# Kernel tuning notes

Measured on AMD Instinct MI355X. Metric: run time of the kernel, lower is better.

Reference implementation:

```python
import jax, jax.numpy as jnp
import numpy as np

B, G, K, C, NT = 128, 64, 32, 256, 8192


def setup_inputs() -> dict:
    key = jax.random.key(0)
    ks = jax.random.split(key, 8)
    s = lambda fan_in: 1.0 / np.sqrt(fan_in)
    return {
        "patch_features": jax.random.normal(ks[0], (B, G, C), jnp.float32),
        "neighborhood": jax.random.normal(ks[1], (B, G, K, 3), jnp.float32),
        "codebook": jax.random.normal(ks[2], (NT, C), jnp.float32),
        "w1": jax.random.normal(ks[3], (512, C), jnp.float32) * s(C),
        "b1": jnp.zeros((512,), jnp.float32),
        "w2": jax.random.normal(ks[4], (256, 512), jnp.float32) * s(512),
        "b2": jnp.zeros((256,), jnp.float32),
        "w3": jax.random.normal(ks[5], (3 * K, 256), jnp.float32) * s(256),
        "b3": jnp.zeros((3 * K,), jnp.float32),
    }


def reference(patch_features, neighborhood, codebook, w1, b1, w2, b2, w3, b3):
    b, g, c = patch_features.shape
    k = neighborhood.shape[2]
    # squared euclidean distances to codebook (argmin equals argmin of cdist p=2)
    d2 = (
        jnp.sum(patch_features * patch_features, -1, keepdims=True)
        - 2.0 * jnp.einsum("bgc,nc->bgn", patch_features, codebook)
        + jnp.sum(codebook * codebook, -1)
    )  # [B,G,NT]
    token_ids = jnp.argmin(d2, axis=-1)          # [B,G]
    quantized = codebook[token_ids]              # [B,G,C] gather
    # 1x1 Conv1d stack == per-token MLP
    h = jax.nn.relu(jnp.einsum("bgc,oc->bgo", quantized, w1) + b1)
    h = jax.nn.relu(jnp.einsum("bgc,oc->bgo", h, w2) + b2)
    rec = jnp.einsum("bgc,oc->bgo", h, w3) + b3  # [B,G,3K]
    rec = rec.reshape(b * g, k, 3)
    gt = neighborhood.reshape(b * g, k, 3)
    # Chamfer distance L2 (squared) both directions
    diff = rec[:, :, None, :] - gt[:, None, :, :]  # [BG,K,K,3]
    dd = jnp.sum(diff * diff, -1)                  # [BG,K,K]
    loss = jnp.mean(jnp.min(dd, axis=2)) + jnp.mean(jnp.min(dd, axis=1))
    return loss
```

## Files before the change

kernel.cpp:

```cpp
#include <hip/hip_runtime.h>
#include <hip/hip_bf16.h>
#include <float.h>

#define NTOK 8192
#define NCB  8192
#define CDIM 256
#define KPTS 32
#define SQNT 24.0f
#define INV_CFOLD (SQNT * SQNT * 64.0f)

typedef __attribute__((ext_vector_type(8))) short short8;
typedef __attribute__((ext_vector_type(4))) float f32x4;
typedef __attribute__((ext_vector_type(4))) int i32x4;
typedef unsigned int u32;
typedef unsigned long long u64;

__device__ __forceinline__ void gl_lds16(const void* g, void* l) {
  __builtin_amdgcn_global_load_lds(
      (const __attribute__((address_space(1))) u32*)(g),
      (__attribute__((address_space(3))) u32*)(l), 16, 0, 0);
}

__device__ __forceinline__ ushort bf16_rne(float x) {
  u32 u = __float_as_uint(x);
  return (ushort)((u + 0x7fffu + ((u >> 16) & 1u)) >> 16);
}

__device__ __forceinline__ int pack4i8(int a, int b, int c, int d) {
  return (a & 0xff) | ((b & 0xff) << 8) | ((c & 0xff) << 16) | ((d & 0xff) << 24);
}

__global__ __launch_bounds__(256) void prep_k(
    const float* __restrict__ pf, const float* __restrict__ cb,
    const float* __restrict__ w1, const float* __restrict__ w2,
    const float* __restrict__ w3,
    i32x4* __restrict__ pf1, i32x4* __restrict__ pf2,
    i32x4* __restrict__ cb1, i32x4* __restrict__ cb2,
    ushort* __restrict__ cb_bf, ushort* __restrict__ w1s,
    ushort* __restrict__ w2s, ushort* __restrict__ w3s,
    float* __restrict__ cnorm) {
  int gid = blockIdx.x * 4 + (threadIdx.x >> 6);
  int lane = threadIdx.x & 63, r16 = lane & 15, quad = lane >> 4;
  if (gid < 4096) {
    bool is_cb = gid >= 2048;
    int t = is_cb ? gid - 2048 : gid;
    int tile = t >> 2, kb = t & 3;
    const float* src = is_cb ? cb : pf;
    int row = tile * 16 + r16;
    const float* sp = src + (size_t)row * CDIM + kb * 64 + quad * 16;
    float4 v0 = ((const float4*)sp)[0];
    float4 v1 = ((const float4*)sp)[1];
    float4 v2 = ((const float4*)sp)[2];
    float4 v3 = ((const float4*)sp)[3];
    float x[16] = {v0.x, v0.y, v0.z, v0.w, v1.x, v1.y, v1.z, v1.w,
                   v2.x, v2.y, v2.z, v2.w, v3.x, v3.y, v3.z, v3.w};
    int q1[16], q2[16];
    float s = 0.f;
#pragma unroll
    for (int e = 0; e < 16; e++) {
      float as = x[e] * SQNT;
      float a1 = rintf(as);
      a1 = fminf(fmaxf(a1, -127.f), 127.f);
      float a2 = rintf((as - a1) * 128.f);
      a2 = fminf(fmaxf(a2, -127.f), 127.f);
      q1[e] = (int)a1;
      q2[e] = (int)a2;
      s += x[e] * x[e];
    }
    i32x4 p1 = {pack4i8(q1[0], q1[1], q1[2], q1[3]),
                pack4i8(q1[4], q1[5], q1[6], q1[7]),
                pack4i8(q1[8], q1[9], q1[10], q1[11]),
                pack4i8(q1[12], q1[13], q1[14], q1[15])};
    i32x4 p2 = {pack4i8(q2[0], q2[1], q2[2], q2[3]),
                pack4i8(q2[4], q2[5], q2[6], q2[7]),
                pack4i8(q2[8], q2[9], q2[10], q2[11]),
                pack4i8(q2[12], q2[13], q2[14], q2[15])};
    size_t o = (size_t)t * 64 + lane;
    (is_cb ? cb1 : pf1)[o] = p1;
    (is_cb ? cb2 : pf2)[o] = p2;
    if (is_cb) {
      s += __shfl_xor(s, 16, 64);
      s += __shfl_xor(s, 32, 64);
      if (quad == 0) atomicAdd(cnorm + row, s);
    }
  } else if (gid < 8192) {
    int t = gid - 4096;
    int tile = t >> 3, kb = t & 7;
    int row = tile * 16 + r16;
    const float* sp = cb + (size_t)row * CDIM + kb * 32 + quad * 8;
    float4 a = ((const float4*)sp)[0];
    float4 b = ((const float4*)sp)[1];
    short8 vh = {(short)bf16_rne(a.x), (short)bf16_rne(a.y),
                 (short)bf16_rne(a.z), (short)bf16_rne(a.w),
                 (short)bf16_rne(b.x), (short)bf16_rne(b.y),
                 (short)bf16_rne(b.z), (short)bf16_rne(b.w)};
    *(short8*)(cb_bf + ((size_t)tile * 8 + kb) * 512 + lane * 8) = vh;
  } else if (gid < 8752) {
    int t = gid - 8192;
    const float* src;
    ushort* dst;
    int KB;
    if (t < 256)      { src = w1; dst = w1s; KB = 8; }
    else if (t < 512) { src = w2; dst = w2s; KB = 16; t -= 256; }
    else              { src = w3; dst = w3s; KB = 8;  t -= 512; }
    int tile = t / KB, kb = t - tile * KB, K = KB * 32;
    int row = tile * 16 + r16;
    const float* sp = src + (size_t)row * K + kb * 32 + quad * 8;
    float4 a = ((const float4*)sp)[0];
    float4 b = ((const float4*)sp)[1];
    short8 vh = {(short)bf16_rne(a.x), (short)bf16_rne(a.y),
                 (short)bf16_rne(a.z), (short)bf16_rne(a.w),
                 (short)bf16_rne(b.x), (short)bf16_rne(b.y),
                 (short)bf16_rne(b.z), (short)bf16_rne(b.w)};
    *(short8*)(dst + ((size_t)tile * KB + kb) * 512 + lane * 8) = vh;
  }
}

__global__ __launch_bounds__(256, 2) void argmin_k(
    const char* __restrict__ A1g, const char* __restrict__ A2g,
    const char* __restrict__ B1g, const char* __restrict__ B2g,
    const float* __restrict__ cnorm, u64* __restrict__ pkeys) {
  __shared__ char lds[32 * 1024];
  int tid = threadIdx.x;
  int ns = blockIdx.x, mt = blockIdx.y;
  int wv = tid >> 6, lane = tid & 63;
  int quad = lane >> 4, r16 = lane & 15;
  int wr = wv >> 1, wc = wv & 1;

  int bvi[4][4], bii[4][4];
#pragma unroll
  for (int i = 0; i < 4; i++)
#pragma unroll
    for (int r = 0; r < 4; r++) { bvi[i][r] = 0x7fffffff; bii[i][r] = 0x7fffffff; }

  const char* bsrc = (wv == 0) ? A1g : (wv == 1) ? A2g : (wv == 2) ? B1g : B2g;

  for (int nts = 0; nts < 4; ++nts) {
    int nt = ns * 4 + nts;
    i32x4 am[4][4], ac[4][4];
#pragma unroll
    for (int i = 0; i < 4; i++)
#pragma unroll
      for (int j = 0; j < 4; j++) {
        am[i][j] = (i32x4){0, 0, 0, 0};
        ac[i][j] = (i32x4){0, 0, 0, 0};
      }
    for (int kb = 0; kb < 4; ++kb) {
#pragma unroll
      for (int u = 0; u < 8; ++u) {
        int gt = ((wv < 2) ? mt : nt) * 8 + u;
        gl_lds16(bsrc + ((size_t)gt * 4 + kb) * 1024 + lane * 16,
                 lds + (wv * 8 + u) * 1024);
      }
      __syncthreads();
      i32x4 f1[4], f2[4], g1[4], g2[4];
#pragma unroll
      for (int i = 0; i < 4; i++) {
        f1[i] = *(const i32x4*)(lds + (wr * 4 + i) * 1024 + lane * 16);
        f2[i] = *(const i32x4*)(lds + (8 + wr * 4 + i) * 1024 + lane * 16);
      }
#pragma unroll
      for (int j = 0; j < 4; j++) {
        g1[j] = *(const i32x4*)(lds + (16 + wc * 4 + j) * 1024 + lane * 16);
        g2[j] = *(const i32x4*)(lds + (24 + wc * 4 + j) * 1024 + lane * 16);
      }
#pragma unroll
      for (int i = 0; i < 4; i++)
#pragma unroll
        for (int j = 0; j < 4; j++) {
          am[i][j] = __builtin_amdgcn_mfma_i32_16x16x64_i8(f1[i], g1[j], am[i][j], 0, 0, 0);
          ac[i][j] = __builtin_amdgcn_mfma_i32_16x16x64_i8(f1[i], g2[j], ac[i][j], 0, 0, 0);
          ac[i][j] = __builtin_amdgcn_mfma_i32_16x16x64_i8(f2[i], g1[j], ac[i][j], 0, 0, 0);
        }
      __syncthreads();
    }
#pragma unroll
    for (int j = 0; j < 4; j++) {
      int col = nt * 128 + wc * 64 + j * 16 + r16;
      int cni = __float2int_rn(cnorm[col] * INV_CFOLD);
#pragma unroll
      for (int i = 0; i < 4; i++)
#pragma unroll
        for (int r = 0; r < 4; r++) {
          int di = cni - (am[i][j][r] * 128 + ac[i][j][r]);
          if (di < bvi[i][r]) { bvi[i][r] = di; bii[i][r] = col; }
        }
    }
  }
#pragma unroll
  for (int m = 1; m < 16; m <<= 1) {
#pragma unroll
    for (int i = 0; i < 4; i++)
#pragma unroll
      for (int r = 0; r < 4; r++) {
        int ov = __shfl_xor(bvi[i][r], m, 64);
        int oi = __shfl_xor(bii[i][r], m, 64);
        if (ov < bvi[i][r] || (ov == bvi[i][r] && oi < bii[i][r])) {
          bvi[i][r] = ov;
          bii[i][r] = oi;
        }
      }
  }
  if (r16 == 0) {
#pragma unroll
    for (int i = 0; i < 4; i++)
#pragma unroll
      for (int r = 0; r < 4; r++) {
        int row = mt * 128 + wr * 64 + i * 16 + quad * 4 + r;
        u32 mk = (u32)(bvi[i][r] + (1 << 30));
        pkeys[(size_t)(ns * 2 + wc) * NTOK + row] = ((u64)mk << 32) | (u32)bii[i][r];
      }
  }
}

__global__ __launch_bounds__(256) void mlp_fused_k(
    const u64* __restrict__ pkeys, const ushort* __restrict__ cb_bf,
    const ushort* __restrict__ w1s, const float* __restrict__ b1,
    const ushort* __restrict__ w2s, const float* __restrict__ b2,
    const ushort* __restrict__ w3s, const float* __restrict__ b3,
    const float* __restrict__ neigh, float* __restrict__ out) {
  __shared__ char lds[65536];
  __shared__ int ids[32];
  __shared__ float wsum[4];
  ushort* qsp = (ushort*)lds;
  ushort* h1p = (ushort*)(lds + 16384);
  ushort* h2p = (ushort*)(lds + 49152);
  float* recp = (float*)lds;
  float* gtsp = (float*)(lds + 16384);

  int tid = threadIdx.x;
  int t0 = blockIdx.x * 32;
  int wv = tid >> 6, lane = tid & 63;
  int quad = lane >> 4, r16 = lane & 15;
  int mtile = wv >> 1, nh = wv & 1;

  {
    int row_l = tid >> 3, sl = tid & 7;
    u64 best = ~0ull;
#pragma unroll
    for (int s = 0; s < 4; s++) {
      u64 v = pkeys[(size_t)(sl + s * 8) * NTOK + t0 + row_l];
      if (v < best) best = v;
    }
#pragma unroll
    for (int m = 1; m < 8; m <<= 1) {
      u64 o = __shfl_xor((unsigned long long)best, m, 64);
      if (o < best) best = o;
    }
    if (sl == 0) ids[row_l] = (int)(u32)best;
  }
  __syncthreads();

  {
    int tile_l = wv >> 1, kb0 = (wv & 1) * 4;
    int id = ids[tile_l * 16 + r16];
#pragma unroll
    for (int q = 0; q < 4; q++) {
      int kb = kb0 + q;
      short8 v = *(const short8*)(cb_bf + ((size_t)(id >> 4) * 8 + kb) * 512 +
                                  (size_t)((id & 15) + quad * 16) * 8);
      *(short8*)(qsp + (size_t)(tile_l * 8 + kb) * 512 + lane * 8) = v;
    }
  }
  __syncthreads();

  {
    short8 fa[8];
#pragma unroll
    for (int kb = 0; kb < 8; kb++)
      fa[kb] = *(const short8*)(qsp + (size_t)(mtile * 8 + kb) * 512 + lane * 8);
    for (int jt = nh * 16; jt < nh * 16 + 16; ++jt) {
      f32x4 acc = (f32x4){0.f, 0.f, 0.f, 0.f};
#pragma unroll
      for (int kb = 0; kb < 8; kb++) {
        short8 fb = *(const short8*)(w1s + ((size_t)jt * 8 + kb) * 512 + lane * 8);
        acc = __builtin_amdgcn_mfma_f32_16x16x32_bf16(fa[kb], fb, acc, 0, 0, 0);
      }
      int col = jt * 16 + r16;
      float bj = b1[col];
#pragma unroll
      for (int reg = 0; reg < 4; reg++) {
        int row_l = mtile * 16 + quad * 4 + reg;
        float v = fmaxf(acc[reg] + bj, 0.f);
        size_t o = (size_t)((row_l >> 4) * 16 + (col >> 5)) * 512 +
                   (size_t)(((col >> 3) & 3) * 16 + (row_l & 15)) * 8 + (col & 7);
        h1p[o] = bf16_rne(v);
      }
    }
  }
  __syncthreads();

  {
    short8 fa[16];
#pragma unroll
    for (int kb = 0; kb < 16; kb++)
      fa[kb] = *(const short8*)(h1p + (size_t)(mtile * 16 + kb) * 512 + lane * 8);
    for (int jt = nh * 8; jt < nh * 8 + 8; ++jt) {
      f32x4 acc = (f32x4){0.f, 0.f, 0.f, 0.f};
#pragma unroll
      for (int kb = 0; kb < 16; kb++) {
        short8 fb = *(const short8*)(w2s + ((size_t)jt * 16 + kb) * 512 + lane * 8);
        acc = __builtin_amdgcn_mfma_f32_16x16x32_bf16(fa[kb], fb, acc, 0, 0, 0);
      }
      int col = jt * 16 + r16;
      float bj = b2[col];
#pragma unroll
      for (int reg = 0; reg < 4; reg++) {
        int row_l = mtile * 16 + quad * 4 + reg;
        float v = fmaxf(acc[reg] + bj, 0.f);
        size_t o = (size_t)((row_l >> 4) * 8 + (col >> 5)) * 512 +
                   (size_t)(((col >> 3) & 3) * 16 + (row_l & 15)) * 8 + (col & 7);
        h2p[o] = bf16_rne(v);
      }
    }
  }
  __syncthreads();

#pragma unroll
  for (int s = 0; s < 3; s++) {
    int idx = tid + s * 256;
    int t = idx / 24, c = (idx - t * 24) * 4;
    *(float4*)(gtsp + (size_t)t * 96 + c) =
        *(const float4*)(neigh + (size_t)(t0 + t) * 96 + c);
  }

  {
    short8 fa[8];
#pragma unroll
    for (int kb = 0; kb < 8; kb++)
      fa[kb] = *(const short8*)(h2p + (size_t)(mtile * 8 + kb) * 512 + lane * 8);
#pragma unroll
    for (int jj = 0; jj < 3; ++jj) {
      int jt = nh * 3 + jj;
      f32x4 acc = (f32x4){0.f, 0.f, 0.f, 0.f};
#pragma unroll
      for (int kb = 0; kb < 8; kb++) {
        short8 fb = *(const short8*)(w3s + ((size_t)jt * 8 + kb) * 512 + lane * 8);
        acc = __builtin_amdgcn_mfma_f32_16x16x32_bf16(fa[kb], fb, acc, 0, 0, 0);
      }
      int col = jt * 16 + r16;
      float bj = b3[col];
#pragma unroll
      for (int reg = 0; reg < 4; reg++) {
        int row_l = mtile * 16 + quad * 4 + reg;
        recp[(size_t)row_l * 96 + col] = acc[reg] + bj;
      }
    }
  }
  __syncthreads();

  float local = 0.f;
#pragma unroll
  for (int pp = 0; pp < 4; ++pp) {
    int p = tid + pp * 256;
    int t = p >> 5, i = p & 31;
    float rx = recp[t * 96 + 3 * i], ry = recp[t * 96 + 3 * i + 1], rz = recp[t * 96 + 3 * i + 2];
    float gx = gtsp[t * 96 + 3 * i], gy = gtsp[t * 96 + 3 * i + 1], gz = gtsp[t * 96 + 3 * i + 2];
    float mA = FLT_MAX, mB = FLT_MAX;
#pragma unroll
    for (int j = 0; j < 32; j++) {
      float dx = rx - gtsp[t * 96 + 3 * j], dy = ry - gtsp[t * 96 + 3 * j + 1],
            dz = rz - gtsp[t * 96 + 3 * j + 2];
      float d = dx * dx + dy * dy + dz * dz;
      mA = fminf(mA, d);
      dx = recp[t * 96 + 3 * j] - gx; dy = recp[t * 96 + 3 * j + 1] - gy;
      dz = recp[t * 96 + 3 * j + 2] - gz;
      d = dx * dx + dy * dy + dz * dz;
      mB = fminf(mB, d);
    }
    local += mA + mB;
  }
#pragma unroll
  for (int off = 32; off; off >>= 1) local += __shfl_down(local, off, 64);
  if ((tid & 63) == 0) wsum[tid >> 6] = local;
  __syncthreads();
  if (tid == 0) {
    float s = wsum[0] + wsum[1] + wsum[2] + wsum[3];
    atomicAdd(out, s * (1.0f / (float)(NTOK * KPTS)));
  }
}

extern "C" void kernel_launch(void* const* d_in, const int* in_sizes, int n_in,
                              void* d_out, int out_size, void* d_ws, size_t ws_size,
                              hipStream_t stream) {
  const float* pf    = (const float*)d_in[0];
  const float* neigh = (const float*)d_in[1];
  const float* cb    = (const float*)d_in[2];
  const float* w1    = (const float*)d_in[3];
  const float* b1    = (const float*)d_in[4];
  const float* w2    = (const float*)d_in[5];
  const float* b2    = (const float*)d_in[6];
  const float* w3    = (const float*)d_in[7];
  const float* b3    = (const float*)d_in[8];
  float* out = (float*)d_out;
  char* base = (char*)d_ws;

  u64*   pkeys = (u64*)base;
  float* cnorm = (float*)(base + 0x200000);
  char*  pf1   = base + 0x210000;
  char*  pf2   = base + 0x410000;
  char*  cb1   = base + 0x610000;
  char*  cb2   = base + 0x810000;
  ushort* cb_bf = (ushort*)(base + 0xA10000);
  ushort* w1s   = (ushort*)(base + 0xE10000);
  ushort* w2s   = (ushort*)(base + 0xE50000);
  ushort* w3s   = (ushort*)(base + 0xE90000);

  hipMemsetAsync(d_out, 0, sizeof(float), stream);
  hipMemsetAsync(cnorm, 0, NCB * sizeof(float), stream);
  prep_k<<<2188, 256, 0, stream>>>(pf, cb, w1, w2, w3,
                                   (i32x4*)pf1, (i32x4*)pf2, (i32x4*)cb1,
                                   (i32x4*)cb2, cb_bf, w1s, w2s, w3s, cnorm);
  argmin_k<<<dim3(16, 64), 256, 0, stream>>>(pf1, pf2, cb1, cb2, cnorm, pkeys);
  mlp_fused_k<<<256, 256, 0, stream>>>(pkeys, cb_bf, w1s, b1, w2s, b2, w3s, b3,
                                       neigh, out);
}
```

Before: 170.0 us.

## Stream MLP weights through double-buffered LDS with async global-to-LDS loads

The fused MLP kernel stops having each wave read weight fragments directly from global memory. It instead merges all three layers into one 35-step loop that prefetches the next weight chunk into a double-buffered LDS region with global_load_lds, while the waves compute MFMAs on the current chunk. LDS is re-laid out so activation, reconstruction and ground-truth buffers alias regions that are no longer live, and dynamic shared memory grows to about 80 KB. The aim is to hide weight-load latency and share each weight load across waves, at the cost of a barrier every step and higher LDS use per block.

```diff
diff --git a/kernel.cpp b/kernel.cpp
--- a/kernel.cpp
+++ b/kernel.cpp
@@ -219,20 +219,20 @@
     const ushort* __restrict__ w2s, const float* __restrict__ b2,
     const ushort* __restrict__ w3s, const float* __restrict__ b3,
     const float* __restrict__ neigh, float* __restrict__ out) {
-  __shared__ char lds[65536];
-  __shared__ int ids[32];
-  __shared__ float wsum[4];
+  extern __shared__ char lds[];
   ushort* qsp = (ushort*)lds;
+  ushort* h2p = (ushort*)lds;
   ushort* h1p = (ushort*)(lds + 16384);
-  ushort* h2p = (ushort*)(lds + 49152);
-  float* recp = (float*)lds;
-  float* gtsp = (float*)(lds + 16384);
+  float* recp = (float*)(lds + 16384);
+  float* gtsp = (float*)(lds + 28672);
+  int* ids = (int*)(lds + 81920);
+  float* wsum = (float*)(lds + 82048);
 
   int tid = threadIdx.x;
   int t0 = blockIdx.x * 32;
   int wv = tid >> 6, lane = tid & 63;
   int quad = lane >> 4, r16 = lane & 15;
-  int mtile = wv >> 1, nh = wv & 1;
+  int mtile = wv & 1, p = wv >> 1;
 
   {
     int row_l = tid >> 3, sl = tid & 7;
@@ -262,19 +262,46 @@
       *(short8*)(qsp + (size_t)(tile_l * 8 + kb) * 512 + lane * 8) = v;
     }
   }
+
+  auto stage_unit = [&](int u) {
+    char* dstbase = lds + 49152 + ((u & 1) << 14);
+#pragma unroll
+    for (int uu = 0; uu < 4; ++uu) {
+      int c = wv + uu * 4;
+      int pj = c >> 3, kb = c & 7;
+      const ushort* src;
+      if (u < 16) {
+        src = w1s + (size_t)((2 * u + pj) * 8 + kb) * 512;
+      } else if (u < 32) {
+        int s2 = u - 16, pair = s2 >> 1, half = s2 & 1;
+        src = w2s + (size_t)((2 * pair + pj) * 16 + half * 8 + kb) * 512;
+      } else {
+        int s3 = u - 32;
+        src = w3s + (size_t)((2 * s3 + pj) * 8 + kb) * 512;
+      }
+      gl_lds16(src + lane * 8, dstbase + pj * 8192 + kb * 1024);
+    }
+  };
+
+  stage_unit(0);
   __syncthreads();
 
-  {
-    short8 fa[8];
-#pragma unroll
-    for (int kb = 0; kb < 8; kb++)
-      fa[kb] = *(const short8*)(qsp + (size_t)(mtile * 8 + kb) * 512 + lane * 8);
-    for (int jt = nh * 16; jt < nh * 16 + 16; ++jt) {
+  short8 fa1[8];
+#pragma unroll
+  for (int kb = 0; kb < 8; kb++)
+    fa1[kb] = *(const short8*)(qsp + (size_t)(mtile * 8 + kb) * 512 + lane * 8);
+
+  f32x4 acc2 = (f32x4){0.f, 0.f, 0.f, 0.f};
+  for (int u = 0; u < 35; ++u) {
+    if (u + 1 < 35) stage_unit(u + 1);
+    const char* wb = lds + 49152 + ((u & 1) << 14) + p * 8192;
+    if (u < 16) {
+      int jt = 2 * u + p;
       f32x4 acc = (f32x4){0.f, 0.f, 0.f, 0.f};
 #pragma unroll
-      for (int kb = 0; kb < 8; kb++) {
-        short8 fb = *(const short8*)(w1s + ((size_t)jt * 8 + kb) * 512 + lane * 8);
-        acc = __builtin_amdgcn_mfma_f32_16x16x32_bf16(fa[kb], fb, acc, 0, 0, 0);
+      for (int q = 0; q < 8; q++) {
+        short8 fb = *(const short8*)(wb + q * 1024 + lane * 16);
+        acc = __builtin_amdgcn_mfma_f32_16x16x32_bf16(fa1[q], fb, acc, 0, 0, 0);
       }
       int col = jt * 16 + r16;
       float bj = b1[col];
@@ -286,57 +313,37 @@
                    (size_t)(((col >> 3) & 3) * 16 + (row_l & 15)) * 8 + (col & 7);
         h1p[o] = bf16_rne(v);
       }
-    }
-  }
-  __syncthreads();
-
-  {
-    short8 fa[16];
-#pragma unroll
-    for (int kb = 0; kb < 16; kb++)
-      fa[kb] = *(const short8*)(h1p + (size_t)(mtile * 16 + kb) * 512 + lane * 8);
-    for (int jt = nh * 8; jt < nh * 8 + 8; ++jt) {
+    } else if (u < 32) {
+      int s2 = u - 16, pair = s2 >> 1, half = s2 & 1;
+      int jt = 2 * pair + p;
+      if (half == 0) acc2 = (f32x4){0.f, 0.f, 0.f, 0.f};
+#pragma unroll
+      for (int q = 0; q < 8; q++) {
+        short8 fa = *(const short8*)(h1p + (size_t)(mtile * 16 + half * 8 + q) * 512 + lane * 8);
+        short8 fb = *(const short8*)(wb + q * 1024 + lane * 16);
+        acc2 = __builtin_amdgcn_mfma_f32_16x16x32_bf16(fa, fb, acc2, 0, 0, 0);
+      }
+      if (half == 1) {
+        int col = jt * 16 + r16;
+        float bj = b2[col];
+#pragma unroll
+        for (int reg = 0; reg < 4; reg++) {
+          int row_l = mtile * 16 + quad * 4 + reg;
+          float v = fmaxf(acc2[reg] + bj, 0.f);
+          size_t o = (size_t)((row_l >> 4) * 8 + (col >> 5)) * 512 +
+                     (size_t)(((col >> 3) & 3) * 16 + (row_l & 15)) * 8 + (col & 7);
+          h2p[o] = bf16_rne(v);
+        }
+      }
+    } else {
+      int s3 = u - 32;
+      int jt = 2 * s3 + p;
       f32x4 acc = (f32x4){0.f, 0.f, 0.f, 0.f};
 #pragma unroll
-      for (int kb = 0; kb < 16; kb++) {
-        short8 fb = *(const short8*)(w2s + ((size_t)jt * 16 + kb) * 512 + lane * 8);
-        acc = __builtin_amdgcn_mfma_f32_16x16x32_bf16(fa[kb], fb, acc, 0, 0, 0);
-      }
-      int col = jt * 16 + r16;
-      float bj = b2[col];
-#pragma unroll
-      for (int reg = 0; reg < 4; reg++) {
-        int row_l = mtile * 16 + quad * 4 + reg;
-        float v = fmaxf(acc[reg] + bj, 0.f);
-        size_t o = (size_t)((row_l >> 4) * 8 + (col >> 5)) * 512 +
-                   (size_t)(((col >> 3) & 3) * 16 + (row_l & 15)) * 8 + (col & 7);
-        h2p[o] = bf16_rne(v);
-      }
-    }
-  }
-  __syncthreads();
-
-#pragma unroll
-  for (int s = 0; s < 3; s++) {
-    int idx = tid + s * 256;
-    int t = idx / 24, c = (idx - t * 24) * 4;
-    *(float4*)(gtsp + (size_t)t * 96 + c) =
-        *(const float4*)(neigh + (size_t)(t0 + t) * 96 + c);
-  }
-
-  {
-    short8 fa[8];
-#pragma unroll
-    for (int kb = 0; kb < 8; kb++)
-      fa[kb] = *(const short8*)(h2p + (size_t)(mtile * 8 + kb) * 512 + lane * 8);
-#pragma unroll
-    for (int jj = 0; jj < 3; ++jj) {
-      int jt = nh * 3 + jj;
-      f32x4 acc = (f32x4){0.f, 0.f, 0.f, 0.f};
-#pragma unroll
-      for (int kb = 0; kb < 8; kb++) {
-        short8 fb = *(const short8*)(w3s + ((size_t)jt * 8 + kb) * 512 + lane * 8);
-        acc = __builtin_amdgcn_mfma_f32_16x16x32_bf16(fa[kb], fb, acc, 0, 0, 0);
+      for (int q = 0; q < 8; q++) {
+        short8 fa = *(const short8*)(h2p + (size_t)(mtile * 8 + q) * 512 + lane * 8);
+        short8 fb = *(const short8*)(wb + q * 1024 + lane * 16);
+        acc = __builtin_amdgcn_mfma_f32_16x16x32_bf16(fa, fb, acc, 0, 0, 0);
       }
       int col = jt * 16 + r16;
       float bj = b3[col];
@@ -345,15 +352,19 @@
         int row_l = mtile * 16 + quad * 4 + reg;
         recp[(size_t)row_l * 96 + col] = acc[reg] + bj;
       }
-    }
-  }
-  __syncthreads();
+      int idx = tid + s3 * 256;
+      int t = idx / 24, c = (idx - t * 24) * 4;
+      *(float4*)(gtsp + (size_t)t * 96 + c) =
+          *(const float4*)(neigh + (size_t)(t0 + t) * 96 + c);
+    }
+    __syncthreads();
+  }
 
   float local = 0.f;
 #pragma unroll
   for (int pp = 0; pp < 4; ++pp) {
-    int p = tid + pp * 256;
-    int t = p >> 5, i = p & 31;
+    int pidx = tid + pp * 256;
+    int t = pidx >> 5, i = pidx & 31;
     float rx = recp[t * 96 + 3 * i], ry = recp[t * 96 + 3 * i + 1], rz = recp[t * 96 + 3 * i + 2];
     float gx = gtsp[t * 96 + 3 * i], gy = gtsp[t * 96 + 3 * i + 1], gz = gtsp[t * 96 + 3 * i + 2];
     float mA = FLT_MAX, mB = FLT_MAX;
@@ -412,6 +423,6 @@
                                    (i32x4*)pf1, (i32x4*)pf2, (i32x4*)cb1,
                                    (i32x4*)cb2, cb_bf, w1s, w2s, w3s, cnorm);
   argmin_k<<<dim3(16, 64), 256, 0, stream>>>(pf1, pf2, cb1, cb2, cnorm, pkeys);
-  mlp_fused_k<<<256, 256, 0, stream>>>(pkeys, cb_bf, w1s, b1, w2s, b2, w3s, b3,
-                                       neigh, out);
-}
+  mlp_fused_k<<<256, 256, 82176, stream>>>(pkeys, cb_bf, w1s, b1, w2s, b2,
+                                           w3s, b3, neigh, out);
+}
```

Result: slower. 185.2 us (+8.9%).

## Double-buffer argmin LDS loads and re-tile MLP kernel to 16 tokens per block

Applied to the files above, without the earlier changes.

The argmin kernel now double-buffers its LDS tiles. It issues global-to-LDS loads for the next k-step before computing the current one, which cuts the barriers per step from two to one and overlaps loads with MFMA work. The fused MLP kernel now processes 16 tokens per block with 512 threads across 512 blocks instead of 32 tokens with 256 threads. This spreads the MLP matmuls across more waves and more CUs. The trade-offs are doubled LDS in argmin, which may lower occupancy, and weight reloads duplicated across more blocks in the MLP.

```diff
diff --git a/kernel.cpp b/kernel.cpp
--- a/kernel.cpp
+++ b/kernel.cpp
@@ -120,7 +120,7 @@
     const char* __restrict__ A1g, const char* __restrict__ A2g,
     const char* __restrict__ B1g, const char* __restrict__ B2g,
     const float* __restrict__ cnorm, u64* __restrict__ pkeys) {
-  __shared__ char lds[32 * 1024];
+  __shared__ char lds[2][32768];
   int tid = threadIdx.x;
   int ns = blockIdx.x, mt = blockIdx.y;
   int wv = tid >> 6, lane = tid & 63;
@@ -135,57 +135,69 @@
 
   const char* bsrc = (wv == 0) ? A1g : (wv == 1) ? A2g : (wv == 2) ? B1g : B2g;
 
-  for (int nts = 0; nts < 4; ++nts) {
+  i32x4 am[4][4], ac[4][4];
+
+  auto stage = [&](int s) {
+    int nts = s >> 2, kb = s & 3;
     int nt = ns * 4 + nts;
-    i32x4 am[4][4], ac[4][4];
+    char* dst = lds[s & 1] + wv * 8192;
+    int gt0 = ((wv < 2) ? mt : nt) * 8;
+#pragma unroll
+    for (int u = 0; u < 8; ++u)
+      gl_lds16(bsrc + ((size_t)(gt0 + u) * 4 + kb) * 1024 + lane * 16,
+               dst + u * 1024);
+  };
+
+  stage(0);
+  __syncthreads();
+  for (int s = 0; s < 16; ++s) {
+    int kb = s & 3, nts = s >> 2;
+    if (kb == 0) {
+#pragma unroll
+      for (int i = 0; i < 4; i++)
+#pragma unroll
+        for (int j = 0; j < 4; j++) {
+          am[i][j] = (i32x4){0, 0, 0, 0};
+          ac[i][j] = (i32x4){0, 0, 0, 0};
+        }
+    }
+    if (s < 15) stage(s + 1);
+    const char* L = lds[s & 1];
+    i32x4 f1[4], f2[4], g1[4], g2[4];
+#pragma unroll
+    for (int i = 0; i < 4; i++) {
+      f1[i] = *(const i32x4*)(L + (wr * 4 + i) * 1024 + lane * 16);
+      f2[i] = *(const i32x4*)(L + (8 + wr * 4 + i) * 1024 + lane * 16);
+    }
+#pragma unroll
+    for (int j = 0; j < 4; j++) {
+      g1[j] = *(const i32x4*)(L + (16 + wc * 4 + j) * 1024 + lane * 16);
+      g2[j] = *(const i32x4*)(L + (24 + wc * 4 + j) * 1024 + lane * 16);
+    }
 #pragma unroll
     for (int i = 0; i < 4; i++)
 #pragma unroll
       for (int j = 0; j < 4; j++) {
-        am[i][j] = (i32x4){0, 0, 0, 0};
-        ac[i][j] = (i32x4){0, 0, 0, 0};
+        am[i][j] = __builtin_amdgcn_mfma_i32_16x16x64_i8(f1[i], g1[j], am[i][j], 0, 0, 0);
+        ac[i][j] = __builtin_amdgcn_mfma_i32_16x16x64_i8(f1[i], g2[j], ac[i][j], 0, 0, 0);
+        ac[i][j] = __builtin_amdgcn_mfma_i32_16x16x64_i8(f2[i], g1[j], ac[i][j], 0, 0, 0);
       }
-    for (int kb = 0; kb < 4; ++kb) {
-#pragma unroll
-      for (int u = 0; u < 8; ++u) {
-        int gt = ((wv < 2) ? mt : nt) * 8 + u;
-        gl_lds16(bsrc + ((size_t)gt * 4 + kb) * 1024 + lane * 16,
-                 lds + (wv * 8 + u) * 1024);
+    if (kb == 3) {
+      int nt = ns * 4 + nts;
+#pragma unroll
+      for (int j = 0; j < 4; j++) {
+        int col = nt * 128 + wc * 64 + j * 16 + r16;
+        int cni = __float2int_rn(cnorm[col] * INV_CFOLD);
+#pragma unroll
+        for (int i = 0; i < 4; i++)
+#pragma unroll
+          for (int r = 0; r < 4; r++) {
+            int di = cni - (am[i][j][r] * 128 + ac[i][j][r]);
+            if (di < bvi[i][r]) { bvi[i][r] = di; bii[i][r] = col; }
+          }
       }
-      __syncthreads();
-      i32x4 f1[4], f2[4], g1[4], g2[4];
-#pragma unroll
-      for (int i = 0; i < 4; i++) {
-        f1[i] = *(const i32x4*)(lds + (wr * 4 + i) * 1024 + lane * 16);
-        f2[i] = *(const i32x4*)(lds + (8 + wr * 4 + i) * 1024 + lane * 16);
-      }
-#pragma unroll
-      for (int j = 0; j < 4; j++) {
-        g1[j] = *(const i32x4*)(lds + (16 + wc * 4 + j) * 1024 + lane * 16);
-        g2[j] = *(const i32x4*)(lds + (24 + wc * 4 + j) * 1024 + lane * 16);
-      }
-#pragma unroll
-      for (int i = 0; i < 4; i++)
-#pragma unroll
-        for (int j = 0; j < 4; j++) {
-          am[i][j] = __builtin_amdgcn_mfma_i32_16x16x64_i8(f1[i], g1[j], am[i][j], 0, 0, 0);
-          ac[i][j] = __builtin_amdgcn_mfma_i32_16x16x64_i8(f1[i], g2[j], ac[i][j], 0, 0, 0);
-          ac[i][j] = __builtin_amdgcn_mfma_i32_16x16x64_i8(f2[i], g1[j], ac[i][j], 0, 0, 0);
-        }
-      __syncthreads();
-    }
-#pragma unroll
-    for (int j = 0; j < 4; j++) {
-      int col = nt * 128 + wc * 64 + j * 16 + r16;
-      int cni = __float2int_rn(cnorm[col] * INV_CFOLD);
-#pragma unroll
-      for (int i = 0; i < 4; i++)
-#pragma unroll
-        for (int r = 0; r < 4; r++) {
-          int di = cni - (am[i][j][r] * 128 + ac[i][j][r]);
-          if (di < bvi[i][r]) { bvi[i][r] = di; bii[i][r] = col; }
-        }
-    }
+    }
+    __syncthreads();
   }
 #pragma unroll
   for (int m = 1; m < 16; m <<= 1) {
@@ -213,37 +225,29 @@
   }
 }
 
-__global__ __launch_bounds__(256) void mlp_fused_k(
+__global__ __launch_bounds__(512) void mlp_fused_k(
     const u64* __restrict__ pkeys, const ushort* __restrict__ cb_bf,
     const ushort* __restrict__ w1s, const float* __restrict__ b1,
     const ushort* __restrict__ w2s, const float* __restrict__ b2,
     const ushort* __restrict__ w3s, const float* __restrict__ b3,
     const float* __restrict__ neigh, float* __restrict__ out) {
-  __shared__ char lds[65536];
-  __shared__ int ids[32];
-  __shared__ float wsum[4];
-  ushort* qsp = (ushort*)lds;
-  ushort* h1p = (ushort*)(lds + 16384);
-  ushort* h2p = (ushort*)(lds + 49152);
-  float* recp = (float*)lds;
-  float* gtsp = (float*)(lds + 16384);
+  __shared__ ushort qs_h2[8 * 512];
+  __shared__ ushort h1s[16 * 512];
+  __shared__ float rec[16 * 96];
+  __shared__ float gts[16 * 96];
+  __shared__ int ids[16];
+  __shared__ float wsum[8];
 
   int tid = threadIdx.x;
-  int t0 = blockIdx.x * 32;
+  int t0 = blockIdx.x * 16;
   int wv = tid >> 6, lane = tid & 63;
   int quad = lane >> 4, r16 = lane & 15;
-  int mtile = wv >> 1, nh = wv & 1;
 
   {
-    int row_l = tid >> 3, sl = tid & 7;
-    u64 best = ~0ull;
-#pragma unroll
-    for (int s = 0; s < 4; s++) {
-      u64 v = pkeys[(size_t)(sl + s * 8) * NTOK + t0 + row_l];
-      if (v < best) best = v;
-    }
-#pragma unroll
-    for (int m = 1; m < 8; m <<= 1) {
+    int row_l = tid >> 5, sl = tid & 31;
+    u64 best = pkeys[(size_t)sl * NTOK + t0 + row_l];
+#pragma unroll
+    for (int m = 1; m < 32; m <<= 1) {
       u64 o = __shfl_xor((unsigned long long)best, m, 64);
       if (o < best) best = o;
     }
@@ -252,130 +256,117 @@
   __syncthreads();
 
   {
-    int tile_l = wv >> 1, kb0 = (wv & 1) * 4;
-    int id = ids[tile_l * 16 + r16];
-#pragma unroll
-    for (int q = 0; q < 4; q++) {
-      int kb = kb0 + q;
-      short8 v = *(const short8*)(cb_bf + ((size_t)(id >> 4) * 8 + kb) * 512 +
-                                  (size_t)((id & 15) + quad * 16) * 8);
-      *(short8*)(qsp + (size_t)(tile_l * 8 + kb) * 512 + lane * 8) = v;
-    }
-  }
-  __syncthreads();
-
+    int kb = wv;
+    int id = ids[r16];
+    short8 v = *(const short8*)(cb_bf + ((size_t)(id >> 4) * 8 + kb) * 512 +
+                                (size_t)((id & 15) + quad * 16) * 8);
+    *(short8*)(qs_h2 + (size_t)kb * 512 + lane * 8) = v;
+  }
+  __syncthreads();
+
+  short8 fa1[8];
+#pragma unroll
+  for (int kb = 0; kb < 8; kb++)
+    fa1[kb] = *(const short8*)(qs_h2 + (size_t)kb * 512 + lane * 8);
+  __syncthreads();
+
+#pragma unroll
+  for (int jj = 0; jj < 4; ++jj) {
+    int jt = wv + jj * 8;
+    f32x4 acc = (f32x4){0.f, 0.f, 0.f, 0.f};
+#pragma unroll
+    for (int kb = 0; kb < 8; kb++) {
+      short8 fb = *(const short8*)(w1s + ((size_t)jt * 8 + kb) * 512 + lane * 8);
+      acc = __builtin_amdgcn_mfma_f32_16x16x32_bf16(fa1[kb], fb, acc, 0, 0, 0);
+    }
+    int col = jt * 16 + r16;
+    float bj = b1[col];
+#pragma unroll
+    for (int reg = 0; reg < 4; reg++) {
+      int row_l = quad * 4 + reg;
+      float v = fmaxf(acc[reg] + bj, 0.f);
+      size_t o = (size_t)(col >> 5) * 512 +
+                 (size_t)(((col >> 3) & 3) * 16 + row_l) * 8 + (col & 7);
+      h1s[o] = bf16_rne(v);
+    }
+  }
+  __syncthreads();
+
+#pragma unroll
+  for (int jj = 0; jj < 2; ++jj) {
+    int jt = wv + jj * 8;
+    f32x4 acc = (f32x4){0.f, 0.f, 0.f, 0.f};
+#pragma unroll
+    for (int kb = 0; kb < 16; kb++) {
+      short8 fa = *(const short8*)(h1s + (size_t)kb * 512 + lane * 8);
+      short8 fb = *(const short8*)(w2s + ((size_t)jt * 16 + kb) * 512 + lane * 8);
+      acc = __builtin_amdgcn_mfma_f32_16x16x32_bf16(fa, fb, acc, 0, 0, 0);
+    }
+    int col = jt * 16 + r16;
+    float bj = b2[col];
+#pragma unroll
+    for (int reg = 0; reg < 4; reg++) {
+      int row_l = quad * 4 + reg;
+      float v = fmaxf(acc[reg] + bj, 0.f);
+      size_t o = (size_t)(col >> 5) * 512 +
+                 (size_t)(((col >> 3) & 3) * 16 + row_l) * 8 + (col & 7);
+      qs_h2[o] = bf16_rne(v);
+    }
+  }
+  __syncthreads();
+
+  if (tid < 384) {
+    int t = tid / 24, c = (tid - t * 24) * 4;
+    *(float4*)(gts + (size_t)t * 96 + c) =
+        *(const float4*)(neigh + (size_t)(t0 + t) * 96 + c);
+  }
+
+  if (wv < 6) {
+    int jt = wv;
+    f32x4 acc = (f32x4){0.f, 0.f, 0.f, 0.f};
+#pragma unroll
+    for (int kb = 0; kb < 8; kb++) {
+      short8 fa = *(const short8*)(qs_h2 + (size_t)kb * 512 + lane * 8);
+      short8 fb = *(const short8*)(w3s + ((size_t)jt * 8 + kb) * 512 + lane * 8);
+      acc = __builtin_amdgcn_mfma_f32_16x16x32_bf16(fa, fb, acc, 0, 0, 0);
+    }
+    int col = jt * 16 + r16;
+    float bj = b3[col];
+#pragma unroll
+    for (int reg = 0; reg < 4; reg++) {
+      int row_l = quad * 4 + reg;
+      rec[(size_t)row_l * 96 + col] = acc[reg] + bj;
+    }
+  }
+  __syncthreads();
+
+  float local = 0.f;
   {
-    short8 fa[8];
-#pragma unroll
-    for (int kb = 0; kb < 8; kb++)
-      fa[kb] = *(const short8*)(qsp + (size_t)(mtile * 8 + kb) * 512 + lane * 8);
-    for (int jt = nh * 16; jt < nh * 16 + 16; ++jt) {
-      f32x4 acc = (f32x4){0.f, 0.f, 0.f, 0.f};
-#pragma unroll
-      for (int kb = 0; kb < 8; kb++) {
-        short8 fb = *(const short8*)(w1s + ((size_t)jt * 8 + kb) * 512 + lane * 8);
-        acc = __builtin_amdgcn_mfma_f32_16x16x32_bf16(fa[kb], fb, acc, 0, 0, 0);
-      }
-      int col = jt * 16 + r16;
-      float bj = b1[col];
-#pragma unroll
-      for (int reg = 0; reg < 4; reg++) {
-        int row_l = mtile * 16 + quad * 4 + reg;
-        float v = fmaxf(acc[reg] + bj, 0.f);
-        size_t o = (size_t)((row_l >> 4) * 16 + (col >> 5)) * 512 +
-                   (size_t)(((col >> 3) & 3) * 16 + (row_l & 15)) * 8 + (col & 7);
-        h1p[o] = bf16_rne(v);
-      }
-    }
-  }
-  __syncthreads();
-
-  {
-    short8 fa[16];
-#pragma unroll
-    for (int kb = 0; kb < 16; kb++)
-      fa[kb] = *(const short8*)(h1p + (size_t)(mtile * 16 + kb) * 512 + lane * 8);
-    for (int jt = nh * 8; jt < nh * 8 + 8; ++jt) {
-      f32x4 acc = (f32x4){0.f, 0.f, 0.f, 0.f};
-#pragma unroll
-      for (int kb = 0; kb < 16; kb++) {
-        short8 fb = *(const short8*)(w2s + ((size_t)jt * 16 + kb) * 512 + lane * 8);
-        acc = __builtin_amdgcn_mfma_f32_16x16x32_bf16(fa[kb], fb, acc, 0, 0, 0);
-      }
-      int col = jt * 16 + r16;
-      float bj = b2[col];
-#pragma unroll
-      for (int reg = 0; reg < 4; reg++) {
-        int row_l = mtile * 16 + quad * 4 + reg;
-        float v = fmaxf(acc[reg] + bj, 0.f);
-        size_t o = (size_t)((row_l >> 4) * 8 + (col >> 5)) * 512 +
-                   (size_t)(((col >> 3) & 3) * 16 + (row_l & 15)) * 8 + (col & 7);
-        h2p[o] = bf16_rne(v);
-      }
-    }
-  }
-  __syncthreads();
-
-#pragma unroll
-  for (int s = 0; s < 3; s++) {
-    int idx = tid + s * 256;
-    int t = idx / 24, c = (idx - t * 24) * 4;
-    *(float4*)(gtsp + (size_t)t * 96 + c) =
-        *(const float4*)(neigh + (size_t)(t0 + t) * 96 + c);
-  }
-
-  {
-    short8 fa[8];
-#pragma unroll
-    for (int kb = 0; kb < 8; kb++)
-      fa[kb] = *(const short8*)(h2p + (size_t)(mtile * 8 + kb) * 512 + lane * 8);
-#pragma unroll
-    for (int jj = 0; jj < 3; ++jj) {
-      int jt = nh * 3 + jj;
-      f32x4 acc = (f32x4){0.f, 0.f, 0.f, 0.f};
-#pragma unroll
-      for (int kb = 0; kb < 8; kb++) {
-        short8 fb = *(const short8*)(w3s + ((size_t)jt * 8 + kb) * 512 + lane * 8);
-        acc = __builtin_amdgcn_mfma_f32_16x16x32_bf16(fa[kb], fb, acc, 0, 0, 0);
-      }
-      int col = jt * 16 + r16;
-      float bj = b3[col];
-#pragma unroll
-      for (int reg = 0; reg < 4; reg++) {
-        int row_l = mtile * 16 + quad * 4 + reg;
-        recp[(size_t)row_l * 96 + col] = acc[reg] + bj;
-      }
-    }
-  }
-  __syncthreads();
-
-  float local = 0.f;
-#pragma unroll
-  for (int pp = 0; pp < 4; ++pp) {
-    int p = tid + pp * 256;
-    int t = p >> 5, i = p & 31;
-    float rx = recp[t * 96 + 3 * i], ry = recp[t * 96 + 3 * i + 1], rz = recp[t * 96 + 3 * i + 2];
-    float gx = gtsp[t * 96 + 3 * i], gy = gtsp[t * 96 + 3 * i + 1], gz = gtsp[t * 96 + 3 * i + 2];
+    int t = tid >> 5, i = tid & 31;
+    float rx = rec[t * 96 + 3 * i], ry = rec[t * 96 + 3 * i + 1], rz = rec[t * 96 + 3 * i + 2];
+    float gx = gts[t * 96 + 3 * i], gy = gts[t * 96 + 3 * i + 1], gz = gts[t * 96 + 3 * i + 2];
     float mA = FLT_MAX, mB = FLT_MAX;
 #pragma unroll
     for (int j = 0; j < 32; j++) {
-      float dx = rx - gtsp[t * 96 + 3 * j], dy = ry - gtsp[t * 96 + 3 * j + 1],
-            dz = rz - gtsp[t * 96 + 3 * j + 2];
+      float dx = rx - gts[t * 96 + 3 * j], dy = ry - gts[t * 96 + 3 * j + 1],
+            dz = rz - gts[t * 96 + 3 * j + 2];
       float d = dx * dx + dy * dy + dz * dz;
       mA = fminf(mA, d);
-      dx = recp[t * 96 + 3 * j] - gx; dy = recp[t * 96 + 3 * j + 1] - gy;
-      dz = recp[t * 96 + 3 * j + 2] - gz;
+      dx = rec[t * 96 + 3 * j] - gx; dy = rec[t * 96 + 3 * j + 1] - gy;
+      dz = rec[t * 96 + 3 * j + 2] - gz;
       d = dx * dx + dy * dy + dz * dz;
       mB = fminf(mB, d);
     }
-    local += mA + mB;
+    local = mA + mB;
   }
 #pragma unroll
   for (int off = 32; off; off >>= 1) local += __shfl_down(local, off, 64);
-  if ((tid & 63) == 0) wsum[tid >> 6] = local;
+  if (lane == 0) wsum[wv] = local;
   __syncthreads();
   if (tid == 0) {
-    float s = wsum[0] + wsum[1] + wsum[2] + wsum[3];
+    float s = 0.f;
+#pragma unroll
+    for (int w = 0; w < 8; w++) s += wsum[w];
     atomicAdd(out, s * (1.0f / (float)(NTOK * KPTS)));
   }
 }
@@ -412,6 +403,6 @@
                                    (i32x4*)pf1, (i32x4*)pf2, (i32x4*)cb1,
                                    (i32x4*)cb2, cb_bf, w1s, w2s, w3s, cnorm);
   argmin_k<<<dim3(16, 64), 256, 0, stream>>>(pf1, pf2, cb1, cb2, cnorm, pkeys);
-  mlp_fused_k<<<256, 256, 0, stream>>>(pkeys, cb_bf, w1s, b1, w2s, b2, w3s, b3,
-                                       neigh, out);
-}
+  mlp_fused_k<<<512, 512, 0, stream>>>(pkeys, cb_bf, w1s, b1, w2s, b2,
+                                       w3s, b3, neigh, out);
+}
```

Result: no change. 167.0 us (-1.8%).
